# Optimization experiments

Measured on AMD Instinct MI355X. Metric: run time of the kernel, lower is better.

The kernel has to match this reference:

```python
import jax, jax.numpy as jnp
import numpy as np

NEG_INF = jnp.float32(-jnp.inf)


def setup_inputs() -> dict:
    key = jax.random.key(0)
    k1, k2, k3, k4 = jax.random.split(key, 4)
    B, T, E = 8, 2048, 1024
    H_DK = 1024  # dk * num_heads
    scale = 1.0 / np.sqrt(E)
    x = jax.random.normal(k1, (B, T, E), dtype=jnp.float32)
    Wq = jax.random.normal(k2, (E, H_DK), dtype=jnp.float32) * scale
    Wk = jax.random.normal(k3, (E, H_DK), dtype=jnp.float32) * scale
    Wv = jax.random.normal(k4, (E, H_DK), dtype=jnp.float32) * scale
    return {"x": x, "Wq": Wq, "Wk": Wk, "Wv": Wv, "dk": 64}


def reference(x, Wq, Wk, Wv, dk):
    # x: [B, T, E]; Wq/Wk/Wv: [E, H*dk] (heads never split in original module)
    Q = jnp.einsum("bte,ed->btd", x, Wq)
    K = jnp.einsum("bte,ed->btd", x, Wk)
    V = jnp.einsum("bte,ed->btd", x, Wv)
    energy = jnp.einsum("bqd,bkd->bqk", Q, K)  # [B, T, T]
    B, T, _ = energy.shape
    # padding mask derived from first query row: lengths[b] = #nonzero of energy[b,0,:]
    lengths = jnp.sum(energy[:, 0] != 0, axis=-1)  # [B]
    j = jnp.arange(T)
    pad_mask = j[None, :] >= lengths[:, None]          # [B, T] -> key positions masked
    causal_mask = j[None, :] > j[:, None]              # [T, T]
    mask = pad_mask[:, None, :] | causal_mask[None, :, :]  # [B, T, T]
    energy = jnp.where(mask, NEG_INF, energy)
    score = jax.nn.softmax(energy / jnp.sqrt(jnp.float32(dk)), axis=-1)
    return jnp.einsum("bqk,bkd->bqd", score, V)
```

## Files before the change

kernel.cpp:

```cpp
#include <hip/hip_runtime.h>

#define DEV __device__ __forceinline__

using f32x4 = __attribute__((ext_vector_type(4))) float;
using f16x8 = __attribute__((ext_vector_type(8))) _Float16;
using f16x4 = __attribute__((ext_vector_type(4))) _Float16;

constexpr int Bc = 8, Tc = 2048, Ec = 1024, Hc = 1024;
constexpr int Mc = Bc * Tc;
constexpr int SLOT = 256 * 32;

DEV f32x4 mfma16(f16x8 a, f16x8 b, f32x4 c) {
    return __builtin_amdgcn_mfma_f32_16x16x32_f16(a, b, c, 0, 0, 0);
}
DEV unsigned short f16bits(float f) { return __builtin_bit_cast(unsigned short, (_Float16)f); }
DEV float f16val(unsigned short u) { return (float)__builtin_bit_cast(_Float16, u); }

DEV void gload16(const _Float16* g, _Float16* l) {
    __builtin_amdgcn_global_load_lds(
        (const __attribute__((address_space(1))) unsigned int*)g,
        (__attribute__((address_space(3))) unsigned int*)l, 16, 0, 0);
}

DEV int swz_off(int R, int lk) {
    return ((R >> 1) << 6) + ((((((R & 1) << 2) | lk) ^ ((R >> 1) & 7))) << 3);
}

__global__ __launch_bounds__(256) void k_prep(const float* __restrict__ x,
                                              const float* __restrict__ wq,
                                              const float* __restrict__ wk,
                                              const float* __restrict__ wv,
                                              _Float16* __restrict__ xf,
                                              _Float16* __restrict__ wall) {
    __shared__ float tile[32][33];
    const int i = blockIdx.x;
    if (i < 16384) {
        const int idx = (i * 256 + threadIdx.x) * 4;
        f32x4 v = *reinterpret_cast<const f32x4*>(x + idx);
        f16x4 h;
#pragma unroll
        for (int j = 0; j < 4; j++) h[j] = (_Float16)v[j];
        *reinterpret_cast<f16x4*>(xf + idx) = h;
    } else {
        const int j = i - 16384;
        const int z = j >> 10;
        const int rem = j & 1023;
        const int n0 = (rem & 31) * 32, e0 = (rem >> 5) * 32;
        const float* src = (z == 0) ? wq : (z == 1) ? wk : wv;
        _Float16* dh = wall + (size_t)z * 1024 * Ec;
        const int tx = threadIdx.x & 31, ty = threadIdx.x >> 5;
#pragma unroll
        for (int jj = 0; jj < 32; jj += 8)
            tile[ty + jj][tx] = src[(size_t)(e0 + ty + jj) * Hc + n0 + tx];
        __syncthreads();
#pragma unroll
        for (int jj = 0; jj < 32; jj += 8)
            dh[(size_t)(n0 + ty + jj) * Ec + e0 + tx] = (_Float16)tile[tx][ty + jj];
    }
}

template <int EPI>
DEV void gemm_body(int bx, int by, int z,
                   const _Float16* __restrict__ Ah, const _Float16* __restrict__ Bh,
                   void* __restrict__ out0, void* __restrict__ out2,
                   const int* __restrict__ dkp,
                   int lda, int ldb, size_t aBS, size_t bBS, size_t oBS, int nkt,
                   _Float16* sAb, _Float16* sBb) {
    if (EPI == 3) nkt = (by + 1) * 8;

    Ah += (size_t)z * aBS;
    Bh += (size_t)z * bBS;

    const float scale = (EPI == 2) ? (1.0f / sqrtf((float)*dkp)) : 1.0f;

    const int tid = threadIdx.x;
    const int wave = tid >> 6, lane = tid & 63;
    const int lr = lane & 15, lk = lane >> 4;
    const int wm = wave >> 2, wn = wave & 3;
    const int m0 = by * 256, n0 = bx * 256;

    const int so = (lane & 7) ^ (lane >> 3);
    const int strow = 2 * (lane >> 3) + (so >> 2);
    const int stcol = (so & 3) * 8;
    const size_t aoff0 = (size_t)(m0 + (wave * 2 + 0) * 16 + strow) * lda + stcol;
    const size_t aoff1 = (size_t)(m0 + (wave * 2 + 1) * 16 + strow) * lda + stcol;
    const size_t boff0 = (size_t)(n0 + (wave * 2 + 0) * 16 + strow) * ldb + stcol;
    const size_t boff1 = (size_t)(n0 + (wave * 2 + 1) * 16 + strow) * ldb + stcol;
    const int ld0 = (wave * 2 + 0) * 512, ld1 = (wave * 2 + 1) * 512;

    auto stage = [&](int sv, int slot) {
        const int kk = sv * 32;
        _Float16* dA = sAb + slot * SLOT;
        _Float16* dB = sBb + slot * SLOT;
        gload16(Ah + aoff0 + kk, dA + ld0);
        gload16(Ah + aoff1 + kk, dA + ld1);
        gload16(Bh + boff0 + kk, dB + ld0);
        gload16(Bh + boff1 + kk, dB + ld1);
    };

    f32x4 acc[8][4] = {};

    stage(0, 0);
    stage(1, 1);
    asm volatile("s_waitcnt vmcnt(4)" ::: "memory");
    __builtin_amdgcn_s_barrier();

    int rP = 0;
    for (int P = 0; P < nkt; ++P) {
        const _Float16* cA = sAb + rP * SLOT;
        const _Float16* cB = sBb + rP * SLOT;
        f16x8 af[8], bfr[4];

#pragma unroll
        for (int nj = 0; nj < 4; nj++)
            bfr[nj] = *reinterpret_cast<const f16x8*>(
                &cB[swz_off(wn * 64 + nj * 16 + lr, lk)]);
#pragma unroll
        for (int mi = 0; mi < 8; mi++)
            af[mi] = *reinterpret_cast<const f16x8*>(
                &cA[swz_off(wm * 128 + mi * 16 + lr, lk)]);

        int rs = rP + 2; if (rs >= 3) rs -= 3;
        if (P + 2 < nkt) stage(P + 2, rs);

        __builtin_amdgcn_s_setprio(1);
#pragma unroll
        for (int mi = 0; mi < 8; mi++)
#pragma unroll
            for (int nj = 0; nj < 4; nj++)
                acc[mi][nj] = mfma16(af[mi], bfr[nj], acc[mi][nj]);
        __builtin_amdgcn_s_setprio(0);

        if (P + 2 < nkt) {
            asm volatile("s_waitcnt vmcnt(4)" ::: "memory");
            __builtin_amdgcn_s_barrier();
        } else if (P + 1 < nkt) {
            asm volatile("s_waitcnt vmcnt(0)" ::: "memory");
            __builtin_amdgcn_s_barrier();
        }
        if (++rP == 3) rP = 0;
    }

#pragma unroll
    for (int mi = 0; mi < 8; mi++)
#pragma unroll
        for (int nj = 0; nj < 4; nj++) {
            const int gn = n0 + wn * 64 + nj * 16 + lr;
            if (EPI == 1) {
                const int gm0 = m0 + wm * 128 + mi * 16 + lk * 4;
                const int bb = gm0 >> 11, t = gm0 & (Tc - 1);
                f16x4 pk;
#pragma unroll
                for (int r = 0; r < 4; r++) pk[r] = (_Float16)acc[mi][nj][r];
                *reinterpret_cast<f16x4*>(
                    &((_Float16*)out0)[((size_t)(bb * Hc + gn)) * Tc + t]) = pk;
            } else if (EPI == 0) {
                _Float16* od = (gn < 1024) ? (_Float16*)out0 : (_Float16*)out2;
                const int cc = gn & 1023;
#pragma unroll
                for (int r = 0; r < 4; r++) {
                    const int gm = m0 + wm * 128 + mi * 16 + lk * 4 + r;
                    od[(size_t)gm * Hc + cc] = (_Float16)acc[mi][nj][r];
                }
            } else {
#pragma unroll
                for (int r = 0; r < 4; r++) {
                    const int gm = m0 + wm * 128 + mi * 16 + lk * 4 + r;
                    const float v = acc[mi][nj][r];
                    if (EPI == 2) {
                        const float e = (gn > gm) ? -INFINITY : v * scale;
                        ((unsigned short*)out0)[(size_t)z * oBS + (size_t)gm * Tc + gn] =
                            f16bits(e);
                    } else {
                        ((float*)out0)[(size_t)z * oBS + (size_t)gm * Hc + gn] = v;
                    }
                }
            }
        }
}

__global__ __launch_bounds__(512, 2) void k_qkv(
        const _Float16* __restrict__ Xf, const _Float16* __restrict__ Wall,
        _Float16* __restrict__ Qf, _Float16* __restrict__ Kf,
        _Float16* __restrict__ Vt, const int* __restrict__ dkp) {
    __shared__ _Float16 sA[3][SLOT];
    __shared__ _Float16 sB[3][SLOT];
    const int i = blockIdx.x;
    if (i < 512) {
        const int w = (i & 7) * 64 + (i >> 3);
        const int by = w >> 3, bx = w & 7;
        gemm_body<0>(bx, by, 0, Xf, Wall, Qf, Kf, dkp,
                     Ec, Ec, 0, 0, 0, 32, sA[0], sB[0]);
    } else {
        const int j = i - 512;
        gemm_body<1>(j & 3, j >> 2, 0, Xf, Wall + (size_t)2048 * Ec,
                     Vt, nullptr, dkp, Ec, Ec, 0, 0, 0, 32, sA[0], sB[0]);
    }
}

__global__ __launch_bounds__(512, 2) void k_energy(
        const _Float16* __restrict__ Qf, const _Float16* __restrict__ Kf,
        unsigned short* __restrict__ S, const int* __restrict__ dkp) {
    __shared__ _Float16 sA[3][SLOT];
    __shared__ _Float16 sB[3][SLOT];
    const int i = blockIdx.x;
    const int b = i / 36;
    int t = i - b * 36;
    int by = 0;
    while (t >= by + 1) { t -= by + 1; by++; }
    gemm_body<2>(t, by, b, Qf, Kf, S, nullptr, dkp,
                 Hc, Hc, (size_t)Tc * Hc, (size_t)Tc * Hc, (size_t)Tc * Tc, 32,
                 sA[0], sB[0]);
}

__global__ __launch_bounds__(512, 2) void k_pv(
        const _Float16* __restrict__ S, const _Float16* __restrict__ Vt,
        float* __restrict__ out, const int* __restrict__ dkp) {
    __shared__ _Float16 sA[3][SLOT];
    __shared__ _Float16 sB[3][SLOT];
    gemm_body<3>(blockIdx.x, blockIdx.y, blockIdx.z, S, Vt, out, nullptr, dkp,
                 Tc, Tc, (size_t)Tc * Tc, (size_t)Hc * Tc, (size_t)Tc * Hc, 0,
                 sA[0], sB[0]);
}

__global__ __launch_bounds__(256) void softmax_w(unsigned short* __restrict__ S) {
    const int rid = blockIdx.x * 4 + (threadIdx.x >> 6);
    const int lane = threadIdx.x & 63;
    const int q = rid & (Tc - 1);
    const int limit = ((q >> 8) + 1) << 8;
    unsigned short* row = S + (size_t)rid * Tc;

    float v[4][8];
    bool act[4];
#pragma unroll
    for (int c = 0; c < 4; c++) {
        const int c0 = c * 512 + lane * 8;
        act[c] = c0 < limit;
        if (act[c]) {
            uint4 raw = *reinterpret_cast<const uint4*>(row + c0);
            unsigned u[4] = {raw.x, raw.y, raw.z, raw.w};
#pragma unroll
            for (int p = 0; p < 4; p++) {
                v[c][2 * p]     = f16val((unsigned short)(u[p] & 0xFFFFu));
                v[c][2 * p + 1] = f16val((unsigned short)(u[p] >> 16));
            }
#pragma unroll
            for (int i = 0; i < 8; i++)
                if (c0 + i > q) v[c][i] = -INFINITY;
        } else {
#pragma unroll
            for (int i = 0; i < 8; i++) v[c][i] = -INFINITY;
        }
    }

    float m = -INFINITY;
#pragma unroll
    for (int c = 0; c < 4; c++)
#pragma unroll
        for (int i = 0; i < 8; i++) m = fmaxf(m, v[c][i]);
#pragma unroll
    for (int off = 1; off < 64; off <<= 1) m = fmaxf(m, __shfl_xor(m, off));

    float s = 0.f;
#pragma unroll
    for (int c = 0; c < 4; c++)
#pragma unroll
        for (int i = 0; i < 8; i++) {
            v[c][i] = __expf(v[c][i] - m);
            s += v[c][i];
        }
#pragma unroll
    for (int off = 1; off < 64; off <<= 1) s += __shfl_xor(s, off);
    const float inv = 1.0f / s;

#pragma unroll
    for (int c = 0; c < 4; c++) {
        if (!act[c]) continue;
        const int c0 = c * 512 + lane * 8;
        unsigned o[4];
#pragma unroll
        for (int p = 0; p < 4; p++) {
            unsigned short a = f16bits(v[c][2 * p] * inv);
            unsigned short bb = f16bits(v[c][2 * p + 1] * inv);
            o[p] = (unsigned)a | ((unsigned)bb << 16);
        }
        uint4 w; w.x = o[0]; w.y = o[1]; w.z = o[2]; w.w = o[3];
        *reinterpret_cast<uint4*>(row + c0) = w;
    }
}

extern "C" void kernel_launch(void* const* d_in, const int* in_sizes, int n_in,
                              void* d_out, int out_size, void* d_ws, size_t ws_size,
                              hipStream_t stream) {
    const float* x  = (const float*)d_in[0];
    const float* Wq = (const float*)d_in[1];
    const float* Wk = (const float*)d_in[2];
    const float* Wv = (const float*)d_in[3];
    const int*   dk = (const int*)d_in[4];
    float* out = (float*)d_out;
    char* ws = (char*)d_ws;

    const size_t SZ_XE = (size_t)Mc * Ec * 2;
    const size_t SZ_W  = (size_t)Ec * Hc * 2;

    size_t o = 0;
    auto nxt = [&](size_t bytes) { void* p = ws + o; o += bytes; return p; };
    _Float16* Qf   = (_Float16*)nxt(SZ_XE);
    _Float16* Kf   = (_Float16*)nxt(SZ_XE);
    _Float16* Vt   = (_Float16*)nxt(SZ_XE);
    _Float16* Xf   = (_Float16*)nxt(SZ_XE);
    _Float16* Wall = (_Float16*)nxt(3 * SZ_W);
    unsigned short* S = (unsigned short*)Xf;
    (void)ws_size; (void)in_sizes; (void)n_in; (void)out_size;

    k_prep<<<19456, 256, 0, stream>>>(x, Wq, Wk, Wv, Xf, Wall);

    k_qkv<<<768, 512, 0, stream>>>(Xf, Wall, Qf, Kf, Vt, dk);

    k_energy<<<288, 512, 0, stream>>>(Qf, Kf, (unsigned short*)S, dk);

    softmax_w<<<Bc * Tc / 4, 256, 0, stream>>>((unsigned short*)S);

    k_pv<<<dim3(4, 8, Bc), 512, 0, stream>>>((const _Float16*)S, Vt, out, dk);
}
```

Baseline: 280.6 us.

## Split long causal PV row-blocks along K with atomic accumulation for balance

The PV GEMM now uses a flat grid where the four heaviest causal row-blocks (by=4..7) are split into two K-halves that accumulate into the output with atomicAdd. The rest run unsplit, and blocks are ordered heaviest-first. The prep kernel gains extra blocks that zero the affected output rows before accumulation. This shortens the critical path from the longest causal tile and improves load balance across CUs. The cost is the atomics, extra zeroing writes, and non-deterministic floating-point summation order.

```diff
diff --git a/kernel.cpp b/kernel.cpp
--- a/kernel.cpp
+++ b/kernel.cpp
@@ -31,7 +31,8 @@
                                               const float* __restrict__ wk,
                                               const float* __restrict__ wv,
                                               _Float16* __restrict__ xf,
-                                              _Float16* __restrict__ wall) {
+                                              _Float16* __restrict__ wall,
+                                              float* __restrict__ out) {
     __shared__ float tile[32][33];
     const int i = blockIdx.x;
     if (i < 16384) {
@@ -41,7 +42,7 @@
 #pragma unroll
         for (int j = 0; j < 4; j++) h[j] = (_Float16)v[j];
         *reinterpret_cast<f16x4*>(xf + idx) = h;
-    } else {
+    } else if (i < 19456) {
         const int j = i - 16384;
         const int z = j >> 10;
         const int rem = j & 1023;
@@ -56,6 +57,11 @@
 #pragma unroll
         for (int jj = 0; jj < 32; jj += 8)
             dh[(size_t)(n0 + ty + jj) * Ec + e0 + tx] = (_Float16)tile[tx][ty + jj];
+    } else {
+        const size_t j = ((size_t)(i - 19456) * 256 + threadIdx.x) * 4;
+        const size_t b = j >> 20, off = j & 1048575;
+        f32x4 zz = {0.f, 0.f, 0.f, 0.f};
+        *reinterpret_cast<f32x4*>(out + b * 2097152 + 1048576 + off) = zz;
     }
 }
 
@@ -64,10 +70,9 @@
                    const _Float16* __restrict__ Ah, const _Float16* __restrict__ Bh,
                    void* __restrict__ out0, void* __restrict__ out2,
                    const int* __restrict__ dkp,
-                   int lda, int ldb, size_t aBS, size_t bBS, size_t oBS, int nkt,
+                   int lda, int ldb, size_t aBS, size_t bBS, size_t oBS,
+                   int kt0, int nkt, int atom,
                    _Float16* sAb, _Float16* sBb) {
-    if (EPI == 3) nkt = (by + 1) * 8;
-
     Ah += (size_t)z * aBS;
     Bh += (size_t)z * bBS;
 
@@ -100,13 +105,13 @@
 
     f32x4 acc[8][4] = {};
 
-    stage(0, 0);
-    stage(1, 1);
+    stage(kt0, 0);
+    stage(kt0 + 1, 1);
     asm volatile("s_waitcnt vmcnt(4)" ::: "memory");
     __builtin_amdgcn_s_barrier();
 
     int rP = 0;
-    for (int P = 0; P < nkt; ++P) {
+    for (int i = 0; i < nkt; ++i) {
         const _Float16* cA = sAb + rP * SLOT;
         const _Float16* cB = sBb + rP * SLOT;
         f16x8 af[8], bfr[4];
@@ -121,7 +126,7 @@
                 &cA[swz_off(wm * 128 + mi * 16 + lr, lk)]);
 
         int rs = rP + 2; if (rs >= 3) rs -= 3;
-        if (P + 2 < nkt) stage(P + 2, rs);
+        if (i + 2 < nkt) stage(kt0 + i + 2, rs);
 
         __builtin_amdgcn_s_setprio(1);
 #pragma unroll
@@ -131,10 +136,10 @@
                 acc[mi][nj] = mfma16(af[mi], bfr[nj], acc[mi][nj]);
         __builtin_amdgcn_s_setprio(0);
 
-        if (P + 2 < nkt) {
+        if (i + 2 < nkt) {
             asm volatile("s_waitcnt vmcnt(4)" ::: "memory");
             __builtin_amdgcn_s_barrier();
-        } else if (P + 1 < nkt) {
+        } else if (i + 1 < nkt) {
             asm volatile("s_waitcnt vmcnt(0)" ::: "memory");
             __builtin_amdgcn_s_barrier();
         }
@@ -172,7 +177,9 @@
                         ((unsigned short*)out0)[(size_t)z * oBS + (size_t)gm * Tc + gn] =
                             f16bits(e);
                     } else {
-                        ((float*)out0)[(size_t)z * oBS + (size_t)gm * Hc + gn] = v;
+                        float* op = (float*)out0 + (size_t)z * oBS + (size_t)gm * Hc + gn;
+                        if (atom) atomicAdd(op, v);
+                        else *op = v;
                     }
                 }
             }
@@ -190,11 +197,11 @@
         const int w = (i & 7) * 64 + (i >> 3);
         const int by = w >> 3, bx = w & 7;
         gemm_body<0>(bx, by, 0, Xf, Wall, Qf, Kf, dkp,
-                     Ec, Ec, 0, 0, 0, 32, sA[0], sB[0]);
+                     Ec, Ec, 0, 0, 0, 0, 32, 0, sA[0], sB[0]);
     } else {
         const int j = i - 512;
         gemm_body<1>(j & 3, j >> 2, 0, Xf, Wall + (size_t)2048 * Ec,
-                     Vt, nullptr, dkp, Ec, Ec, 0, 0, 0, 32, sA[0], sB[0]);
+                     Vt, nullptr, dkp, Ec, Ec, 0, 0, 0, 0, 32, 0, sA[0], sB[0]);
     }
 }
 
@@ -209,8 +216,8 @@
     int by = 0;
     while (t >= by + 1) { t -= by + 1; by++; }
     gemm_body<2>(t, by, b, Qf, Kf, S, nullptr, dkp,
-                 Hc, Hc, (size_t)Tc * Hc, (size_t)Tc * Hc, (size_t)Tc * Tc, 32,
-                 sA[0], sB[0]);
+                 Hc, Hc, (size_t)Tc * Hc, (size_t)Tc * Hc, (size_t)Tc * Tc,
+                 0, 32, 0, sA[0], sB[0]);
 }
 
 __global__ __launch_bounds__(512, 2) void k_pv(
@@ -218,9 +225,20 @@
         float* __restrict__ out, const int* __restrict__ dkp) {
     __shared__ _Float16 sA[3][SLOT];
     __shared__ _Float16 sB[3][SLOT];
-    gemm_body<3>(blockIdx.x, blockIdx.y, blockIdx.z, S, Vt, out, nullptr, dkp,
-                 Tc, Tc, (size_t)Tc * Tc, (size_t)Hc * Tc, (size_t)Tc * Hc, 0,
-                 sA[0], sB[0]);
+    const int i = blockIdx.x;
+    int by, ktn, kt0 = 0, atom = 0, r;
+    if (i < 64)        { by = 7; ktn = 32; r = i;        atom = 1; kt0 = (r & 1) * 32; r >>= 1; }
+    else if (i < 96)   { by = 3; ktn = 32; r = i - 64; }
+    else if (i < 160)  { by = 6; ktn = 28; r = i - 96;   atom = 1; kt0 = (r & 1) * 28; r >>= 1; }
+    else if (i < 224)  { by = 5; ktn = 24; r = i - 160;  atom = 1; kt0 = (r & 1) * 24; r >>= 1; }
+    else if (i < 256)  { by = 2; ktn = 24; r = i - 224; }
+    else if (i < 320)  { by = 4; ktn = 20; r = i - 256;  atom = 1; kt0 = (r & 1) * 20; r >>= 1; }
+    else if (i < 352)  { by = 1; ktn = 16; r = i - 320; }
+    else               { by = 0; ktn = 8;  r = i - 352; }
+    const int bx = r & 3, b = r >> 2;
+    gemm_body<3>(bx, by, b, S, Vt, out, nullptr, dkp,
+                 Tc, Tc, (size_t)Tc * Tc, (size_t)Hc * Tc, (size_t)Tc * Hc,
+                 kt0, ktn, atom, sA[0], sB[0]);
 }
 
 __global__ __launch_bounds__(256) void softmax_w(unsigned short* __restrict__ S) {
@@ -313,7 +331,7 @@
     unsigned short* S = (unsigned short*)Xf;
     (void)ws_size; (void)in_sizes; (void)n_in; (void)out_size;
 
-    k_prep<<<19456, 256, 0, stream>>>(x, Wq, Wk, Wv, Xf, Wall);
+    k_prep<<<27648, 256, 0, stream>>>(x, Wq, Wk, Wv, Xf, Wall, out);
 
     k_qkv<<<768, 512, 0, stream>>>(Xf, Wall, Qf, Kf, Vt, dk);
 
@@ -321,5 +339,5 @@
 
     softmax_w<<<Bc * Tc / 4, 256, 0, stream>>>((unsigned short*)S);
 
-    k_pv<<<dim3(4, 8, Bc), 512, 0, stream>>>((const _Float16*)S, Vt, out, dk);
-}
+    k_pv<<<384, 512, 0, stream>>>((const _Float16*)S, Vt, out, dk);
+}
```

Result: slower. 305.4 us (+8.8%).

## Restructure GEMM mainloop into 64-wide K steps with split-phase interleaved staging

Applied to the files above, without the earlier changes.

Replaces the 3-slot, 32-wide K pipeline with a double-buffered 64-wide K step, where each step runs as four compute phases. Each phase issues a partial A or B global-to-LDS load for upcoming tiles, separated by barriers. This spreads memory issue across MFMA work and halves the number of A fragments held per phase, which may lower register pressure. The cost is more barriers per K step and more complex vmcnt accounting, and LDS use rises from 3 to 4 slots per operand.

```diff
diff --git a/kernel.cpp b/kernel.cpp
--- a/kernel.cpp
+++ b/kernel.cpp
@@ -66,7 +66,7 @@
                    const int* __restrict__ dkp,
                    int lda, int ldb, size_t aBS, size_t bBS, size_t oBS, int nkt,
                    _Float16* sAb, _Float16* sBb) {
-    if (EPI == 3) nkt = (by + 1) * 8;
+    if (EPI == 3) nkt = (by + 1) * 4;
 
     Ah += (size_t)z * aBS;
     Bh += (size_t)z * bBS;
@@ -88,57 +88,99 @@
     const size_t boff1 = (size_t)(n0 + (wave * 2 + 1) * 16 + strow) * ldb + stcol;
     const int ld0 = (wave * 2 + 0) * 512, ld1 = (wave * 2 + 1) * 512;
 
-    auto stage = [&](int sv, int slot) {
-        const int kk = sv * 32;
-        _Float16* dA = sAb + slot * SLOT;
-        _Float16* dB = sBb + slot * SLOT;
+    auto stageA = [&](int sv, int kh) {
+        const int kk = sv * 64 + kh * 32;
+        _Float16* dA = sAb + (size_t)(sv & 1) * (2 * SLOT) + kh * SLOT;
         gload16(Ah + aoff0 + kk, dA + ld0);
         gload16(Ah + aoff1 + kk, dA + ld1);
+    };
+    auto stageB = [&](int sv, int kh) {
+        const int kk = sv * 64 + kh * 32;
+        _Float16* dB = sBb + (size_t)(sv & 1) * (2 * SLOT) + kh * SLOT;
         gload16(Bh + boff0 + kk, dB + ld0);
         gload16(Bh + boff1 + kk, dB + ld1);
     };
 
     f32x4 acc[8][4] = {};
-
-    stage(0, 0);
-    stage(1, 1);
-    asm volatile("s_waitcnt vmcnt(4)" ::: "memory");
+    f16x8 bfr[4];
+
+    stageA(0, 0); stageB(0, 0); stageA(0, 1); stageB(0, 1);
+    stageB(1, 0); stageA(1, 0); stageB(1, 1);
+    asm volatile("s_waitcnt vmcnt(6)" ::: "memory");
     __builtin_amdgcn_s_barrier();
 
-    int rP = 0;
-    for (int P = 0; P < nkt; ++P) {
-        const _Float16* cA = sAb + rP * SLOT;
-        const _Float16* cB = sBb + rP * SLOT;
-        f16x8 af[8], bfr[4];
+    for (int T = 0; T < nkt; ++T) {
+        const _Float16* cA = sAb + (size_t)(T & 1) * (2 * SLOT);
+        const _Float16* cB = sBb + (size_t)(T & 1) * (2 * SLOT);
+        f16x8 af[4];
 
 #pragma unroll
         for (int nj = 0; nj < 4; nj++)
             bfr[nj] = *reinterpret_cast<const f16x8*>(
                 &cB[swz_off(wn * 64 + nj * 16 + lr, lk)]);
 #pragma unroll
-        for (int mi = 0; mi < 8; mi++)
-            af[mi] = *reinterpret_cast<const f16x8*>(
-                &cA[swz_off(wm * 128 + mi * 16 + lr, lk)]);
-
-        int rs = rP + 2; if (rs >= 3) rs -= 3;
-        if (P + 2 < nkt) stage(P + 2, rs);
-
+        for (int i = 0; i < 4; i++)
+            af[i] = *reinterpret_cast<const f16x8*>(
+                &cA[swz_off(wm * 128 + i * 16 + lr, lk)]);
+        if (T + 1 < nkt) stageA(T + 1, 1);
         __builtin_amdgcn_s_setprio(1);
 #pragma unroll
-        for (int mi = 0; mi < 8; mi++)
+        for (int i = 0; i < 4; i++)
 #pragma unroll
             for (int nj = 0; nj < 4; nj++)
-                acc[mi][nj] = mfma16(af[mi], bfr[nj], acc[mi][nj]);
+                acc[i][nj] = mfma16(af[i], bfr[nj], acc[i][nj]);
         __builtin_amdgcn_s_setprio(0);
-
-        if (P + 2 < nkt) {
-            asm volatile("s_waitcnt vmcnt(4)" ::: "memory");
+        __builtin_amdgcn_s_barrier();
+
+#pragma unroll
+        for (int i = 0; i < 4; i++)
+            af[i] = *reinterpret_cast<const f16x8*>(
+                &cA[swz_off(wm * 128 + (i + 4) * 16 + lr, lk)]);
+        if (T + 2 < nkt) stageB(T + 2, 0);
+        __builtin_amdgcn_s_setprio(1);
+#pragma unroll
+        for (int i = 0; i < 4; i++)
+#pragma unroll
+            for (int nj = 0; nj < 4; nj++)
+                acc[i + 4][nj] = mfma16(af[i], bfr[nj], acc[i + 4][nj]);
+        __builtin_amdgcn_s_setprio(0);
+        __builtin_amdgcn_s_barrier();
+
+#pragma unroll
+        for (int nj = 0; nj < 4; nj++)
+            bfr[nj] = *reinterpret_cast<const f16x8*>(
+                &cB[SLOT + swz_off(wn * 64 + nj * 16 + lr, lk)]);
+#pragma unroll
+        for (int i = 0; i < 4; i++)
+            af[i] = *reinterpret_cast<const f16x8*>(
+                &cA[SLOT + swz_off(wm * 128 + i * 16 + lr, lk)]);
+        if (T + 2 < nkt) stageA(T + 2, 0);
+        __builtin_amdgcn_s_setprio(1);
+#pragma unroll
+        for (int i = 0; i < 4; i++)
+#pragma unroll
+            for (int nj = 0; nj < 4; nj++)
+                acc[i][nj] = mfma16(af[i], bfr[nj], acc[i][nj]);
+        __builtin_amdgcn_s_setprio(0);
+        __builtin_amdgcn_s_barrier();
+
+#pragma unroll
+        for (int i = 0; i < 4; i++)
+            af[i] = *reinterpret_cast<const f16x8*>(
+                &cA[SLOT + swz_off(wm * 128 + (i + 4) * 16 + lr, lk)]);
+        if (T + 2 < nkt) stageB(T + 2, 1);
+        __builtin_amdgcn_s_setprio(1);
+#pragma unroll
+        for (int i = 0; i < 4; i++)
+#pragma unroll
+            for (int nj = 0; nj < 4; nj++)
+                acc[i + 4][nj] = mfma16(af[i], bfr[nj], acc[i + 4][nj]);
+        __builtin_amdgcn_s_setprio(0);
+        if (T < nkt - 1) {
+            if (T + 2 < nkt) asm volatile("s_waitcnt vmcnt(6)" ::: "memory");
+            else             asm volatile("s_waitcnt vmcnt(0)" ::: "memory");
             __builtin_amdgcn_s_barrier();
-        } else if (P + 1 < nkt) {
-            asm volatile("s_waitcnt vmcnt(0)" ::: "memory");
-            __builtin_amdgcn_s_barrier();
-        }
-        if (++rP == 3) rP = 0;
+        }
     }
 
 #pragma unroll
@@ -183,44 +225,44 @@
         const _Float16* __restrict__ Xf, const _Float16* __restrict__ Wall,
         _Float16* __restrict__ Qf, _Float16* __restrict__ Kf,
         _Float16* __restrict__ Vt, const int* __restrict__ dkp) {
-    __shared__ _Float16 sA[3][SLOT];
-    __shared__ _Float16 sB[3][SLOT];
+    __shared__ _Float16 sA[2][2][SLOT];
+    __shared__ _Float16 sB[2][2][SLOT];
     const int i = blockIdx.x;
     if (i < 512) {
         const int w = (i & 7) * 64 + (i >> 3);
         const int by = w >> 3, bx = w & 7;
         gemm_body<0>(bx, by, 0, Xf, Wall, Qf, Kf, dkp,
-                     Ec, Ec, 0, 0, 0, 32, sA[0], sB[0]);
+                     Ec, Ec, 0, 0, 0, 16, sA[0][0], sB[0][0]);
     } else {
         const int j = i - 512;
         gemm_body<1>(j & 3, j >> 2, 0, Xf, Wall + (size_t)2048 * Ec,
-                     Vt, nullptr, dkp, Ec, Ec, 0, 0, 0, 32, sA[0], sB[0]);
+                     Vt, nullptr, dkp, Ec, Ec, 0, 0, 0, 16, sA[0][0], sB[0][0]);
     }
 }
 
 __global__ __launch_bounds__(512, 2) void k_energy(
         const _Float16* __restrict__ Qf, const _Float16* __restrict__ Kf,
         unsigned short* __restrict__ S, const int* __restrict__ dkp) {
-    __shared__ _Float16 sA[3][SLOT];
-    __shared__ _Float16 sB[3][SLOT];
+    __shared__ _Float16 sA[2][2][SLOT];
+    __shared__ _Float16 sB[2][2][SLOT];
     const int i = blockIdx.x;
     const int b = i / 36;
     int t = i - b * 36;
     int by = 0;
     while (t >= by + 1) { t -= by + 1; by++; }
     gemm_body<2>(t, by, b, Qf, Kf, S, nullptr, dkp,
-                 Hc, Hc, (size_t)Tc * Hc, (size_t)Tc * Hc, (size_t)Tc * Tc, 32,
-                 sA[0], sB[0]);
+                 Hc, Hc, (size_t)Tc * Hc, (size_t)Tc * Hc, (size_t)Tc * Tc, 16,
+                 sA[0][0], sB[0][0]);
 }
 
 __global__ __launch_bounds__(512, 2) void k_pv(
         const _Float16* __restrict__ S, const _Float16* __restrict__ Vt,
         float* __restrict__ out, const int* __restrict__ dkp) {
-    __shared__ _Float16 sA[3][SLOT];
-    __shared__ _Float16 sB[3][SLOT];
+    __shared__ _Float16 sA[2][2][SLOT];
+    __shared__ _Float16 sB[2][2][SLOT];
     gemm_body<3>(blockIdx.x, blockIdx.y, blockIdx.z, S, Vt, out, nullptr, dkp,
                  Tc, Tc, (size_t)Tc * Tc, (size_t)Hc * Tc, (size_t)Tc * Hc, 0,
-                 sA[0], sB[0]);
+                 sA[0][0], sB[0][0]);
 }
 
 __global__ __launch_bounds__(256) void softmax_w(unsigned short* __restrict__ S) {
```

Measured after the change: 306.5 us. 1.09x slower.
